# Kernel optimization log

Hardware: AMD Instinct MI355X
Metric: run time of the kernel (lower is better)

Reference implementation:

```python
import jax, jax.numpy as jnp
import numpy as np

jax.config.update("jax_enable_x64", True)  # FixedPointMul math is done in float64, as in torch

B, S, H = 8, 4096, 768


def setup_inputs():
    key = jax.random.key(0)
    k = jax.random.split(key, 6)
    s_act = jnp.array([4.0 / 127.0], dtype=jnp.float32)  # per-tensor 8-bit activation scale

    def qact(kk):  # produce int8-quantized-looking activations
        x = jax.random.normal(kk, (B, S, H), jnp.float32)
        return s_act * jnp.clip(jnp.round(x / s_act), -128, 127)

    return {
        "hidden_states": qact(k[0]),
        "hidden_states_scaling_factor": s_act,
        "input_tensor": qact(k[1]),
        "input_tensor_scaling_factor": s_act,
        "dense_weight": 0.02 * jax.random.normal(k[2], (H, H), jnp.float32),
        "dense_bias": 0.01 * jax.random.normal(k[3], (H,), jnp.float32),
        "ln_weight": 1.0 + 0.05 * jax.random.normal(k[4], (H,), jnp.float32),
        "ln_bias": 0.05 * jax.random.normal(k[5], (H,), jnp.float32),
    }


def _sym_scale(k, smin, smax):
    n = 2 ** (k - 1) - 1
    return jnp.clip(jnp.maximum(jnp.abs(smin), jnp.abs(smax)), 1e-8, None) / n


def _sym_quant(x, k, scale):
    n = 2 ** (k - 1) - 1
    return jnp.clip(jnp.round(x / scale), -n, n - 1)


def _batch_frexp(x):
    # returns (round(mantissa * 2^31), 31 - exponent) as in ibert batch_frexp
    m, e = jnp.frexp(x)
    return jnp.floor(m * (2.0 ** 31) + 0.5), 31.0 - e


def _fixedpoint_mul(x, pre_scale, bit, z_scale, identity=None, id_scale=None):
    n = 2 ** (bit - 1) - 1
    ps = jnp.reshape(pre_scale, (1, 1, -1)).astype(jnp.float64)
    z = z_scale.astype(jnp.float64)
    z_int = jnp.round(x.astype(jnp.float64) / ps)
    m, e = _batch_frexp(ps / z)
    out = jnp.round(z_int * m / (2.0 ** e))
    if identity is not None:
        isf = jnp.reshape(id_scale, (1, 1, -1)).astype(jnp.float64)
        wx = jnp.round(identity.astype(jnp.float64) / isf)
        m1, e1 = _batch_frexp(isf / z)
        out = out + jnp.round(wx * m1 / (2.0 ** e1))
    return jnp.clip(out, -n - 1, n).astype(jnp.float32)


def _quant_act(x, bit, pre_scale, identity=None, id_scale=None):
    x_act = x if identity is None else x + identity
    s = _sym_scale(bit, x_act.min(), x_act.max())  # per-tensor scale (dynamic range)
    q = _fixedpoint_mul(x, pre_scale, bit, s, identity, id_scale)
    return q * s, s


def reference(hidden_states, hidden_states_scaling_factor, input_tensor, input_tensor_scaling_factor, dense_weight, dense_bias, ln_weight, ln_bias):
    # ---- QuantLinear: per-channel int8 weights, int32 bias ----
    w_min = dense_weight.min(axis=1)
    w_max = dense_weight.max(axis=1)
    fc_scale = _sym_scale(8, w_min, w_max)                      # [H_out]
    w_int = _sym_quant(dense_weight, 8, fc_scale[:, None])      # [H_out, H_in]
    bias_scale = fc_scale * hidden_states_scaling_factor        # [H_out]
    b_int = _sym_quant(dense_bias, 32, bias_scale)
    x_int = hidden_states / hidden_states_scaling_factor
    hs = (jnp.einsum("bsh,oh->bso", x_int, w_int) + b_int) * bias_scale
    # dropout: eval mode -> identity
    # ---- QuantAct(22-bit) with quantized residual add ----
    hs, ln_in_scale = _quant_act(hs, 22, bias_scale, input_tensor, input_tensor_scaling_factor)
    # ---- IntLayerNorm (integer-only LayerNorm) ----
    x_int = hs / ln_in_scale
    mean_int = jnp.round(jnp.mean(x_int, axis=2, keepdims=True))
    y_int = x_int - mean_int
    var0 = jnp.sum(y_int ** 2, axis=2, keepdims=True)
    shift = jnp.ceil(jnp.log2(jnp.sqrt(jnp.maximum(var0, 1.0) / 2.0 ** 32)))  # set_shift (max_bit=32)
    shift = jnp.maximum(0.0, shift.max())
    y_sh = jnp.floor(y_int / 2.0 ** shift)
    var_int = jnp.sum(y_sh ** 2, axis=2, keepdims=True)
    std_int = jnp.floor(jnp.sqrt(var_int)) * 2.0 ** shift
    factor = jnp.floor(2.0 ** 31 / std_int)
    y_int = jnp.floor(y_int * factor / 2.0)
    sf = jnp.sqrt(jnp.float32(H)) / 2.0 ** 30
    bias_int = jnp.floor((ln_bias / ln_weight) / sf)
    y_int = y_int + bias_int
    sf_out = sf * ln_weight                                     # [H]
    hs = y_int * sf_out
    # ---- QuantAct(8-bit) output requantization ----
    hs, out_scale = _quant_act(hs, 8, sf_out)
    return hs, out_scale
```

## Files before the change

kernel.cpp:

```cpp
#include <hip/hip_runtime.h>

typedef int   v4i   __attribute__((ext_vector_type(4)));
typedef unsigned long u64x2 __attribute__((ext_vector_type(2)));

#define HDIM 768
#define NTOK 32768

static constexpr size_t WX_OFF   = 0;
static constexpr size_t WINT_OFF = 25165824;
static constexpr size_t RS1_OFF  = WINT_OFF + 1179648;
static constexpr size_t RS2_OFF  = RS1_OFF + 6144;
static constexpr size_t BS_OFF   = RS2_OFF + 6144;
static constexpr size_t BINT_OFF = BS_OFF + 3072;
static constexpr size_t LNBI_OFF = BINT_OFF + 3072;
static constexpr size_t SFO_OFF  = LNBI_OFF + 3072;
static constexpr size_t SC_OFF   = SFO_OFF + 3072;
static constexpr size_t RSM1_OFF = SC_OFF + 64;

__device__ __forceinline__ unsigned fenc(float f) {
    unsigned u = __float_as_uint(f);
    return (u >> 31) ? ~u : (u | 0x80000000u);
}
__device__ __forceinline__ float fdec(unsigned e) {
    unsigned u = (e >> 31) ? (e & 0x7fffffffu) : ~e;
    return __uint_as_float(u);
}

#define GLDS16(g, l) __builtin_amdgcn_global_load_lds( \
    (const __attribute__((address_space(1))) unsigned int*)(g), \
    (__attribute__((address_space(3))) unsigned int*)(l), 16, 0, 0)

__device__ __forceinline__ int swz4(int r) { return (r & 3) ^ ((r >> 2) & 3); }

__global__ __launch_bounds__(256) void k0_prep(const float* __restrict__ W,
                                               const float* __restrict__ bias,
                                               const float* __restrict__ ln_w,
                                               const float* __restrict__ ln_b,
                                               const float* __restrict__ phsf,
                                               char* __restrict__ ws) {
    int o = blockIdx.x, tid = threadIdx.x;
    __shared__ float red[256];
    __shared__ float fc_sh;
    float m = 0.f;
    for (int j = tid; j < HDIM; j += 256) m = fmaxf(m, fabsf(W[(size_t)o * HDIM + j]));
    red[tid] = m;
    __syncthreads();
    for (int s = 128; s; s >>= 1) { if (tid < s) red[tid] = fmaxf(red[tid], red[tid + s]); __syncthreads(); }
    if (tid == 0) {
        float fc = fmaxf(red[0], 1e-8f) / 127.0f;
        float hsf = *phsf;
        float bs = fc * hsf;
        fc_sh = fc;
        ((float*)(ws + BS_OFF))[o] = bs;
        ((int*)(ws + BINT_OFF))[o] = (int)rintf(bias[o] / bs);
        float sf = sqrtf(768.0f) / 1073741824.0f;
        float lw = ln_w[o], lb = ln_b[o];
        ((int*)(ws + LNBI_OFF))[o] = (int)floorf((lb / lw) / sf);
        ((float*)(ws + SFO_OFF))[o] = sf * lw;
    }
    __syncthreads();
    float fc = fc_sh;
    char* w8 = (char*)(ws + WINT_OFF);
    for (int j = tid; j < HDIM; j += 256) {
        float q = rintf(W[(size_t)o * HDIM + j] / fc);
        q = fminf(fmaxf(q, -127.f), 126.f);
        w8[(size_t)o * HDIM + j] = (char)q;
    }
    if (blockIdx.x == 0 && tid < 8) {
        unsigned* sc = (unsigned*)(ws + SC_OFF);
        unsigned v = 0u;
        if (tid == 0 || tid == 2) v = 0xFFFFFFFFu;
        sc[tid] = v;
    }
}

__global__ __launch_bounds__(256) void kp_a8(const float* __restrict__ hs,
                                             const float* __restrict__ phsf,
                                             char* __restrict__ ws) {
    int idx = blockIdx.x * 256 + threadIdx.x;
    float inv = 1.0f / *phsf;
    const float4* in4 = (const float4*)hs + (size_t)idx * 4;
    unsigned ow[4];
    #pragma unroll
    for (int j = 0; j < 4; ++j) {
        float4 v = in4[j];
        int q0 = (int)rintf(v.x * inv), q1 = (int)rintf(v.y * inv);
        int q2 = (int)rintf(v.z * inv), q3 = (int)rintf(v.w * inv);
        ow[j] = (unsigned)(q0 & 255) | ((unsigned)(q1 & 255) << 8) |
                ((unsigned)(q2 & 255) << 16) | ((unsigned)(q3 & 255) << 24);
    }
    ((uint4*)(ws + WX_OFF))[idx] = make_uint4(ow[0], ow[1], ow[2], ow[3]);
}

#define BM 128
#define BN 192
#define BK 64
#define NKT (HDIM / BK)
__global__ __launch_bounds__(256) void k1_gemm(const float* __restrict__ inp,
                                               char* __restrict__ ws,
                                               int* __restrict__ accOut) {
    __shared__ alignas(16) char As[2][BM * BK];
    __shared__ alignas(16) char Bs[2][BN * BK];
    __shared__ float rmn[4], rmx[4];
    int tid = threadIdx.x, lane = tid & 63, wave = tid >> 6;
    int wrow = lane & 15, g = lane >> 4;
    int bid = blockIdx.x;
    int xcd = bid & 7, slot = bid >> 3;
    int mtile = xcd * 32 + (slot >> 2);
    int ntile = slot & 3;
    int t0 = mtile * BM, o0 = ntile * BN;
    const char* a8 = (const char*)(ws + WX_OFF);
    const char* w8 = (const char*)(ws + WINT_OFF);

    const char* asrc[2]; const char* bsrc[3];
    int aldso[2], bldso[3];
    #pragma unroll
    for (int i = 0; i < 2; ++i) {
        int c = i * 256 + tid, r = c >> 2, s = c & 3;
        asrc[i] = a8 + (size_t)(t0 + r) * HDIM + (s ^ swz4(r)) * 16;
        aldso[i] = (i * 256 + wave * 64) * 16;
    }
    #pragma unroll
    for (int i = 0; i < 3; ++i) {
        int c = i * 256 + tid, r = c >> 2, s = c & 3;
        bsrc[i] = w8 + (size_t)(o0 + r) * HDIM + (s ^ swz4(r)) * 16;
        bldso[i] = (i * 256 + wave * 64) * 16;
    }

    int wm = wave & 1, wn = wave >> 1;
    int aofs[4], bofs[6];
    #pragma unroll
    for (int mi = 0; mi < 4; ++mi) { int r = wm * 64 + mi * 16 + wrow; aofs[mi] = r * BK + ((g ^ swz4(r)) * 16); }
    #pragma unroll
    for (int nf = 0; nf < 6; ++nf) { int r = wn * 96 + nf * 16 + wrow; bofs[nf] = r * BK + ((g ^ swz4(r)) * 16); }

    #pragma unroll
    for (int i = 0; i < 2; ++i) GLDS16(asrc[i], &As[0][aldso[i]]);
    #pragma unroll
    for (int i = 0; i < 3; ++i) GLDS16(bsrc[i], &Bs[0][bldso[i]]);
    #pragma unroll
    for (int i = 0; i < 2; ++i) GLDS16(asrc[i] + BK, &As[1][aldso[i]]);
    #pragma unroll
    for (int i = 0; i < 3; ++i) GLDS16(bsrc[i] + BK, &Bs[1][bldso[i]]);
    asm volatile("s_waitcnt vmcnt(5)" ::: "memory");
    __builtin_amdgcn_s_barrier();

    v4i acc[4][6] = {};
    for (int kt = 0; kt < NKT; ++kt) {
        int cur = kt & 1;
        u64x2 af[4], bf[6];
        #pragma unroll
        for (int mi = 0; mi < 4; ++mi) af[mi] = *(const u64x2*)&As[cur][aofs[mi]];
        #pragma unroll
        for (int nf = 0; nf < 6; ++nf) bf[nf] = *(const u64x2*)&Bs[cur][bofs[nf]];
        asm volatile("s_waitcnt lgkmcnt(0)" ::: "memory");
        __builtin_amdgcn_s_barrier();
        if (kt + 2 < NKT) {
            #pragma unroll
            for (int i = 0; i < 2; ++i) GLDS16(asrc[i] + (kt + 2) * BK, &As[cur][aldso[i]]);
            #pragma unroll
            for (int i = 0; i < 3; ++i) GLDS16(bsrc[i] + (kt + 2) * BK, &Bs[cur][bldso[i]]);
        }
        __builtin_amdgcn_s_setprio(1);
        #pragma unroll
        for (int mi = 0; mi < 4; ++mi)
            #pragma unroll
            for (int nf = 0; nf < 6; ++nf) {
                acc[mi][nf] = __builtin_amdgcn_mfma_i32_16x16x32_i8((long)af[mi][0], (long)bf[nf][0], acc[mi][nf], 0, 0, 0);
                acc[mi][nf] = __builtin_amdgcn_mfma_i32_16x16x32_i8((long)af[mi][1], (long)bf[nf][1], acc[mi][nf], 0, 0, 0);
            }
        __builtin_amdgcn_s_setprio(0);
        if (kt + 2 < NKT) {
            asm volatile("s_waitcnt vmcnt(5)" ::: "memory");
            __builtin_amdgcn_s_barrier();
        } else if (kt + 2 == NKT) {
            asm volatile("s_waitcnt vmcnt(0)" ::: "memory");
            __builtin_amdgcn_s_barrier();
        }
    }

    const float* bscale = (const float*)(ws + BS_OFF);
    const int* bint = (const int*)(ws + BINT_OFF);
    int oo[6]; float bsc[6]; int bi[6];
    #pragma unroll
    for (int nf = 0; nf < 6; ++nf) {
        oo[nf] = o0 + wn * 96 + nf * 16 + wrow;
        bsc[nf] = bscale[oo[nf]];
        bi[nf]  = bint[oo[nf]];
    }
    float lmn = 3.402823466e38f, lmx = -3.402823466e38f;
    #pragma unroll
    for (int mi = 0; mi < 4; ++mi)
        #pragma unroll
        for (int r = 0; r < 4; ++r) {
            int t = t0 + wm * 64 + mi * 16 + g * 4 + r;
            size_t rb = (size_t)t * HDIM;
            #pragma unroll
            for (int nf = 0; nf < 6; ++nf) {
                int a = acc[mi][nf][r] + bi[nf];
                size_t idx = rb + oo[nf];
                accOut[idx] = a;
                float xa = (float)a * bsc[nf] + inp[idx];
                lmn = fminf(lmn, xa);
                lmx = fmaxf(lmx, xa);
            }
        }
    #pragma unroll
    for (int off = 32; off; off >>= 1) {
        lmn = fminf(lmn, __shfl_down(lmn, off));
        lmx = fmaxf(lmx, __shfl_down(lmx, off));
    }
    if (lane == 0) { rmn[wave] = lmn; rmx[wave] = lmx; }
    __syncthreads();
    if (tid == 0) {
        float mn = fminf(fminf(rmn[0], rmn[1]), fminf(rmn[2], rmn[3]));
        float mx = fmaxf(fmaxf(rmx[0], rmx[1]), fmaxf(rmx[2], rmx[3]));
        volatile unsigned* sc = (volatile unsigned*)(ws + SC_OFF);
        unsigned emn = fenc(mn), emx = fenc(mx);
        if (emn < sc[0]) atomicMin((unsigned*)&sc[0], emn);
        if (emx > sc[1]) atomicMax((unsigned*)&sc[1], emx);
    }
}

__global__ __launch_bounds__(256) void k2_scale1(const float* __restrict__ pisf, char* __restrict__ ws) {
    __shared__ float s_sh;
    unsigned* sc = (unsigned*)(ws + SC_OFF);
    if (threadIdx.x == 0) {
        float mn = fdec(sc[0]), mx = fdec(sc[1]);
        float s = fmaxf(fmaxf(fabsf(mn), fabsf(mx)), 1e-8f) / 2097151.0f;
        ((float*)sc)[5] = s;
        s_sh = s;
        double r = (double)(*pisf) / (double)s;
        int ex; double mant = frexp(r, &ex);
        double m1 = floor(mant * 2147483648.0 + 0.5);
        ((double*)(ws + RSM1_OFF))[0] = m1 * exp2((double)(ex - 31));
    }
    __syncthreads();
    float s = s_sh;
    const float* bs = (const float*)(ws + BS_OFF);
    double* rs1 = (double*)(ws + RS1_OFF);
    for (int o = threadIdx.x; o < HDIM; o += 256) {
        double r = (double)bs[o] / (double)s;
        int ex; double mant = frexp(r, &ex);
        double m = floor(mant * 2147483648.0 + 0.5);
        rs1[o] = m * exp2((double)(ex - 31));
    }
}

__global__ __launch_bounds__(256) void k3_rows(char* __restrict__ ws, int* __restrict__ buf,
                                               const float* __restrict__ inp,
                                               const float* __restrict__ pisf) {
    int tid = threadIdx.x, lane = tid & 63, wave = tid >> 6;
    int wid = blockIdx.x * 4 + wave;
    const double* rs1 = (const double*)(ws + RS1_OFF);
    double rsm1 = *(const double*)(ws + RSM1_OFF);
    float inv_isf = 1.0f / *pisf;
    int localShift = 0;
    int4 aP[3]; float4 xP[3];
    {
        size_t b0 = (size_t)(wid * 4) * HDIM;
        #pragma unroll
        for (int c = 0; c < 3; ++c) {
            aP[c] = ((const int4*)(buf + b0))[lane + 64 * c];
            xP[c] = ((const float4*)(inp + b0))[lane + 64 * c];
        }
    }
    for (int rr = 0; rr < 4; ++rr) {
        int4 aN[3]; float4 xN[3];
        if (rr < 3) {
            size_t nb = (size_t)(wid * 4 + rr + 1) * HDIM;
            #pragma unroll
            for (int c = 0; c < 3; ++c) {
                aN[c] = ((const int4*)(buf + nb))[lane + 64 * c];
                xN[c] = ((const float4*)(inp + nb))[lane + 64 * c];
            }
        }
        size_t base = (size_t)(wid * 4 + rr) * HDIM;
        int q[12];
        int sum = 0;
        #pragma unroll
        for (int c = 0; c < 3; ++c) {
            int o0 = (lane + 64 * c) * 4;
            int av[4] = {aP[c].x, aP[c].y, aP[c].z, aP[c].w};
            float xv[4] = {xP[c].x, xP[c].y, xP[c].z, xP[c].w};
            #pragma unroll
            for (int j = 0; j < 4; ++j) {
                double q1 = rint((double)av[j] * rs1[o0 + j]);
                int wxj = (int)rintf(xv[j] * inv_isf);
                double qq = q1 + rint((double)wxj * rsm1);
                qq = fmin(fmax(qq, -2097152.0), 2097151.0);
                q[c * 4 + j] = (int)qq;
                sum += q[c * 4 + j];
            }
        }
        #pragma unroll
        for (int off = 32; off; off >>= 1) sum += __shfl_xor(sum, off);
        int mean = (int)rint((double)sum / 768.0);
        long long var0 = 0;
        #pragma unroll
        for (int k = 0; k < 12; ++k) { q[k] -= mean; var0 += (long long)q[k] * (long long)q[k]; }
        #pragma unroll
        for (int off = 32; off; off >>= 1) var0 += __shfl_xor(var0, off);
        #pragma unroll
        for (int c = 0; c < 3; ++c) {
            int4 y = {q[c * 4 + 0], q[c * 4 + 1], q[c * 4 + 2], q[c * 4 + 3]};
            ((int4*)(buf + base))[lane + 64 * c] = y;
        }
        if (lane == 0) {
            double v = (double)(var0 < 1 ? 1LL : var0);
            int sr = (int)ceil(0.5 * log2(v) - 16.0);
            localShift = max(localShift, sr);
        }
        #pragma unroll
        for (int c = 0; c < 3; ++c) { aP[c] = aN[c]; xP[c] = xN[c]; }
    }
    if (lane == 0 && localShift > 0) {
        int* sp = (int*)(ws + SC_OFF) + 4;
        if (localShift > *(volatile int*)sp) atomicMax(sp, localShift);
    }
}

__global__ __launch_bounds__(256) void k4_rows(char* __restrict__ ws, int* __restrict__ buf) {
    int tid = threadIdx.x, lane = tid & 63, wave = tid >> 6;
    int wid = blockIdx.x * 4 + wave;
    int shift = *(((const int*)(ws + SC_OFF)) + 4);
    const int* lnbi = (const int*)(ws + LNBI_OFF);
    const float* sfo = (const float*)(ws + SFO_OFF);
    float lmn = 3.402823466e38f, lmx = -3.402823466e38f;
    int4 yP[3];
    {
        size_t b0 = (size_t)(wid * 4) * HDIM;
        #pragma unroll
        for (int c = 0; c < 3; ++c) yP[c] = ((const int4*)(buf + b0))[lane + 64 * c];
    }
    for (int rr = 0; rr < 4; ++rr) {
        int4 yN[3];
        if (rr < 3) {
            size_t nb = (size_t)(wid * 4 + rr + 1) * HDIM;
            #pragma unroll
            for (int c = 0; c < 3; ++c) yN[c] = ((const int4*)(buf + nb))[lane + 64 * c];
        }
        size_t base = (size_t)(wid * 4 + rr) * HDIM;
        int yv[12];
        #pragma unroll
        for (int c = 0; c < 3; ++c) {
            yv[c * 4 + 0] = yP[c].x; yv[c * 4 + 1] = yP[c].y; yv[c * 4 + 2] = yP[c].z; yv[c * 4 + 3] = yP[c].w;
        }
        long long var = 0;
        #pragma unroll
        for (int k = 0; k < 12; ++k) { int ysh = yv[k] >> shift; var += (long long)ysh * (long long)ysh; }
        #pragma unroll
        for (int off = 32; off; off >>= 1) var += __shfl_xor(var, off);
        double std_int = floor(sqrt((double)var)) * (double)(1LL << shift);
        if (std_int < 1.0) std_int = 1.0;
        long long factor = (long long)floor(2147483648.0 / std_int);
        #pragma unroll
        for (int c = 0; c < 3; ++c) {
            int o0 = (lane + 64 * c) * 4;
            int y2[4];
            #pragma unroll
            for (int j = 0; j < 4; ++j) {
                long long t = ((long long)yv[c * 4 + j] * factor) >> 1;
                int v2 = (int)t + lnbi[o0 + j];
                y2[j] = v2;
                float h = (float)v2 * sfo[o0 + j];
                lmn = fminf(lmn, h);
                lmx = fmaxf(lmx, h);
            }
            int4 w = {y2[0], y2[1], y2[2], y2[3]};
            ((int4*)(buf + base))[lane + 64 * c] = w;
        }
        #pragma unroll
        for (int c = 0; c < 3; ++c) yP[c] = yN[c];
    }
    #pragma unroll
    for (int off = 32; off; off >>= 1) {
        lmn = fminf(lmn, __shfl_xor(lmn, off));
        lmx = fmaxf(lmx, __shfl_xor(lmx, off));
    }
    if (lane == 0) {
        volatile unsigned* sc = (volatile unsigned*)(ws + SC_OFF);
        unsigned emn = fenc(lmn), emx = fenc(lmx);
        if (emn < sc[2]) atomicMin((unsigned*)&sc[2], emn);
        if (emx > sc[3]) atomicMax((unsigned*)&sc[3], emx);
    }
}

__global__ __launch_bounds__(256) void k5_scale2(char* __restrict__ ws) {
    __shared__ float s_sh;
    unsigned* sc = (unsigned*)(ws + SC_OFF);
    if (threadIdx.x == 0) {
        float mn = fdec(sc[2]), mx = fdec(sc[3]);
        float s2 = fmaxf(fmaxf(fabsf(mn), fabsf(mx)), 1e-8f) / 127.0f;
        ((float*)sc)[6] = s2;
        s_sh = s2;
    }
    __syncthreads();
    float s2 = s_sh;
    const float* sfo = (const float*)(ws + SFO_OFF);
    double* rs2 = (double*)(ws + RS2_OFF);
    for (int o = threadIdx.x; o < HDIM; o += 256) {
        double r = (double)sfo[o] / (double)s2;
        int ex; double mant = frexp(r, &ex);
        double m = floor(mant * 2147483648.0 + 0.5);
        rs2[o] = m * exp2((double)(ex - 31));
    }
}

__global__ __launch_bounds__(256) void k6_out(char* __restrict__ ws, float* __restrict__ out) {
    int idx4 = blockIdx.x * 256 + threadIdx.x;
    int4 y = ((const int4*)out)[idx4];
    const double* rs2 = (const double*)(ws + RS2_OFF);
    float s2 = ((const float*)(ws + SC_OFF))[6];
    int base = idx4 * 4;
    int o0 = base % HDIM;
    int yv[4] = {y.x, y.y, y.z, y.w};
    float4 r;
    float* rp = &r.x;
    #pragma unroll
    for (int j = 0; j < 4; ++j) {
        double q = rint((double)yv[j] * rs2[o0 + j]);
        q = fmin(fmax(q, -128.0), 127.0);
        rp[j] = (float)q * s2;
    }
    ((float4*)out)[idx4] = r;
    if (idx4 == 0) out[(size_t)NTOK * HDIM] = s2;
}

extern "C" void kernel_launch(void* const* d_in, const int* in_sizes, int n_in,
                              void* d_out, int out_size, void* d_ws, size_t ws_size,
                              hipStream_t stream) {
    const float* hs   = (const float*)d_in[0];
    const float* phsf = (const float*)d_in[1];
    const float* inp  = (const float*)d_in[2];
    const float* pisf = (const float*)d_in[3];
    const float* W    = (const float*)d_in[4];
    const float* bias = (const float*)d_in[5];
    const float* ln_w = (const float*)d_in[6];
    const float* ln_b = (const float*)d_in[7];
    char* ws = (char*)d_ws;
    float* out = (float*)d_out;
    int* buf = (int*)d_out;

    k0_prep<<<HDIM, 256, 0, stream>>>(W, bias, ln_w, ln_b, phsf, ws);
    kp_a8<<<NTOK * HDIM / 4096, 256, 0, stream>>>(hs, phsf, ws);
    k1_gemm<<<(NTOK / BM) * (HDIM / BN), 256, 0, stream>>>(inp, ws, buf);
    k2_scale1<<<1, 256, 0, stream>>>(pisf, ws);
    k3_rows<<<NTOK / 16, 256, 0, stream>>>(ws, buf, inp, pisf);
    k4_rows<<<NTOK / 16, 256, 0, stream>>>(ws, buf);
    k5_scale2<<<1, 256, 0, stream>>>(ws);
    k6_out<<<NTOK * HDIM / 1024, 256, 0, stream>>>(ws, out);
}
```

Measured before the change: 440.1 us.

## Store per-row LN factor instead of rewriting buffer; recompute in output kernel

k4 no longer writes the normalized integer row back to the buffer. It stores one factor per row in workspace, and k6 recomputes y*factor>>1 + bias from the centered values, which removes a full-tensor write pass. k3 and k4 now handle one row per wave instead of four, with four times as many blocks. k4 also reduces min/max within the block through shared memory before issuing atomics. The trade is a little extra integer arithmetic in k6 and more blocks and atomics in k3.

```diff
diff --git a/kernel.cpp b/kernel.cpp
--- a/kernel.cpp
+++ b/kernel.cpp
@@ -8,6 +8,7 @@
 
 static constexpr size_t WX_OFF   = 0;
 static constexpr size_t WINT_OFF = 25165824;
+static constexpr size_t FACT_OFF = WINT_OFF + 589824;
 static constexpr size_t RS1_OFF  = WINT_OFF + 1179648;
 static constexpr size_t RS2_OFF  = RS1_OFF + 6144;
 static constexpr size_t BS_OFF   = RS2_OFF + 6144;
@@ -251,136 +252,107 @@
                                                const float* __restrict__ inp,
                                                const float* __restrict__ pisf) {
     int tid = threadIdx.x, lane = tid & 63, wave = tid >> 6;
-    int wid = blockIdx.x * 4 + wave;
+    int row = blockIdx.x * 4 + wave;
     const double* rs1 = (const double*)(ws + RS1_OFF);
     double rsm1 = *(const double*)(ws + RSM1_OFF);
     float inv_isf = 1.0f / *pisf;
-    int localShift = 0;
-    int4 aP[3]; float4 xP[3];
-    {
-        size_t b0 = (size_t)(wid * 4) * HDIM;
-        #pragma unroll
-        for (int c = 0; c < 3; ++c) {
-            aP[c] = ((const int4*)(buf + b0))[lane + 64 * c];
-            xP[c] = ((const float4*)(inp + b0))[lane + 64 * c];
-        }
-    }
-    for (int rr = 0; rr < 4; ++rr) {
-        int4 aN[3]; float4 xN[3];
-        if (rr < 3) {
-            size_t nb = (size_t)(wid * 4 + rr + 1) * HDIM;
-            #pragma unroll
-            for (int c = 0; c < 3; ++c) {
-                aN[c] = ((const int4*)(buf + nb))[lane + 64 * c];
-                xN[c] = ((const float4*)(inp + nb))[lane + 64 * c];
-            }
-        }
-        size_t base = (size_t)(wid * 4 + rr) * HDIM;
-        int q[12];
-        int sum = 0;
-        #pragma unroll
-        for (int c = 0; c < 3; ++c) {
-            int o0 = (lane + 64 * c) * 4;
-            int av[4] = {aP[c].x, aP[c].y, aP[c].z, aP[c].w};
-            float xv[4] = {xP[c].x, xP[c].y, xP[c].z, xP[c].w};
-            #pragma unroll
-            for (int j = 0; j < 4; ++j) {
-                double q1 = rint((double)av[j] * rs1[o0 + j]);
-                int wxj = (int)rintf(xv[j] * inv_isf);
-                double qq = q1 + rint((double)wxj * rsm1);
-                qq = fmin(fmax(qq, -2097152.0), 2097151.0);
-                q[c * 4 + j] = (int)qq;
-                sum += q[c * 4 + j];
-            }
-        }
-        #pragma unroll
-        for (int off = 32; off; off >>= 1) sum += __shfl_xor(sum, off);
-        int mean = (int)rint((double)sum / 768.0);
-        long long var0 = 0;
-        #pragma unroll
-        for (int k = 0; k < 12; ++k) { q[k] -= mean; var0 += (long long)q[k] * (long long)q[k]; }
-        #pragma unroll
-        for (int off = 32; off; off >>= 1) var0 += __shfl_xor(var0, off);
-        #pragma unroll
-        for (int c = 0; c < 3; ++c) {
-            int4 y = {q[c * 4 + 0], q[c * 4 + 1], q[c * 4 + 2], q[c * 4 + 3]};
-            ((int4*)(buf + base))[lane + 64 * c] = y;
-        }
-        if (lane == 0) {
-            double v = (double)(var0 < 1 ? 1LL : var0);
-            int sr = (int)ceil(0.5 * log2(v) - 16.0);
-            localShift = max(localShift, sr);
-        }
-        #pragma unroll
-        for (int c = 0; c < 3; ++c) { aP[c] = aN[c]; xP[c] = xN[c]; }
-    }
-    if (lane == 0 && localShift > 0) {
-        int* sp = (int*)(ws + SC_OFF) + 4;
-        if (localShift > *(volatile int*)sp) atomicMax(sp, localShift);
-    }
-}
-
-__global__ __launch_bounds__(256) void k4_rows(char* __restrict__ ws, int* __restrict__ buf) {
+    size_t base = (size_t)row * HDIM;
+    int4 a[3]; float4 x[3];
+    #pragma unroll
+    for (int c = 0; c < 3; ++c) {
+        a[c] = ((const int4*)(buf + base))[lane + 64 * c];
+        x[c] = ((const float4*)(inp + base))[lane + 64 * c];
+    }
+    int q[12];
+    int sum = 0;
+    #pragma unroll
+    for (int c = 0; c < 3; ++c) {
+        int o0 = (lane + 64 * c) * 4;
+        int av[4] = {a[c].x, a[c].y, a[c].z, a[c].w};
+        float xv[4] = {x[c].x, x[c].y, x[c].z, x[c].w};
+        #pragma unroll
+        for (int j = 0; j < 4; ++j) {
+            double q1 = rint((double)av[j] * rs1[o0 + j]);
+            int wxj = (int)rintf(xv[j] * inv_isf);
+            double qq = q1 + rint((double)wxj * rsm1);
+            qq = fmin(fmax(qq, -2097152.0), 2097151.0);
+            q[c * 4 + j] = (int)qq;
+            sum += q[c * 4 + j];
+        }
+    }
+    #pragma unroll
+    for (int off = 32; off; off >>= 1) sum += __shfl_xor(sum, off);
+    int mean = (int)rint((double)sum / 768.0);
+    long long var0 = 0;
+    #pragma unroll
+    for (int k = 0; k < 12; ++k) { q[k] -= mean; var0 += (long long)q[k] * (long long)q[k]; }
+    #pragma unroll
+    for (int off = 32; off; off >>= 1) var0 += __shfl_xor(var0, off);
+    #pragma unroll
+    for (int c = 0; c < 3; ++c) {
+        int4 y = {q[c * 4 + 0], q[c * 4 + 1], q[c * 4 + 2], q[c * 4 + 3]};
+        ((int4*)(buf + base))[lane + 64 * c] = y;
+    }
+    if (lane == 0) {
+        double v = (double)(var0 < 1 ? 1LL : var0);
+        int sr = (int)ceil(0.5 * log2(v) - 16.0);
+        if (sr > 0) {
+            int* sp = (int*)(ws + SC_OFF) + 4;
+            if (sr > *(volatile int*)sp) atomicMax(sp, sr);
+        }
+    }
+}
+
+__global__ __launch_bounds__(256) void k4_rows(char* __restrict__ ws, const int* __restrict__ buf) {
     int tid = threadIdx.x, lane = tid & 63, wave = tid >> 6;
-    int wid = blockIdx.x * 4 + wave;
+    int row = blockIdx.x * 4 + wave;
     int shift = *(((const int*)(ws + SC_OFF)) + 4);
     const int* lnbi = (const int*)(ws + LNBI_OFF);
     const float* sfo = (const float*)(ws + SFO_OFF);
+    __shared__ float rmn[4], rmx[4];
+    size_t base = (size_t)row * HDIM;
+    int4 y4[3];
+    #pragma unroll
+    for (int c = 0; c < 3; ++c) y4[c] = ((const int4*)(buf + base))[lane + 64 * c];
+    int yv[12];
+    #pragma unroll
+    for (int c = 0; c < 3; ++c) {
+        yv[c * 4 + 0] = y4[c].x; yv[c * 4 + 1] = y4[c].y; yv[c * 4 + 2] = y4[c].z; yv[c * 4 + 3] = y4[c].w;
+    }
+    long long var = 0;
+    #pragma unroll
+    for (int k = 0; k < 12; ++k) { int ysh = yv[k] >> shift; var += (long long)ysh * (long long)ysh; }
+    #pragma unroll
+    for (int off = 32; off; off >>= 1) var += __shfl_xor(var, off);
+    double std_int = floor(sqrt((double)var)) * (double)(1LL << shift);
+    if (std_int < 1.0) std_int = 1.0;
+    long long factor = (long long)floor(2147483648.0 / std_int);
+    if (lane == 0) ((unsigned*)(ws + FACT_OFF))[row] = (unsigned)factor;
     float lmn = 3.402823466e38f, lmx = -3.402823466e38f;
-    int4 yP[3];
-    {
-        size_t b0 = (size_t)(wid * 4) * HDIM;
-        #pragma unroll
-        for (int c = 0; c < 3; ++c) yP[c] = ((const int4*)(buf + b0))[lane + 64 * c];
-    }
-    for (int rr = 0; rr < 4; ++rr) {
-        int4 yN[3];
-        if (rr < 3) {
-            size_t nb = (size_t)(wid * 4 + rr + 1) * HDIM;
-            #pragma unroll
-            for (int c = 0; c < 3; ++c) yN[c] = ((const int4*)(buf + nb))[lane + 64 * c];
-        }
-        size_t base = (size_t)(wid * 4 + rr) * HDIM;
-        int yv[12];
-        #pragma unroll
-        for (int c = 0; c < 3; ++c) {
-            yv[c * 4 + 0] = yP[c].x; yv[c * 4 + 1] = yP[c].y; yv[c * 4 + 2] = yP[c].z; yv[c * 4 + 3] = yP[c].w;
-        }
-        long long var = 0;
-        #pragma unroll
-        for (int k = 0; k < 12; ++k) { int ysh = yv[k] >> shift; var += (long long)ysh * (long long)ysh; }
-        #pragma unroll
-        for (int off = 32; off; off >>= 1) var += __shfl_xor(var, off);
-        double std_int = floor(sqrt((double)var)) * (double)(1LL << shift);
-        if (std_int < 1.0) std_int = 1.0;
-        long long factor = (long long)floor(2147483648.0 / std_int);
-        #pragma unroll
-        for (int c = 0; c < 3; ++c) {
-            int o0 = (lane + 64 * c) * 4;
-            int y2[4];
-            #pragma unroll
-            for (int j = 0; j < 4; ++j) {
-                long long t = ((long long)yv[c * 4 + j] * factor) >> 1;
-                int v2 = (int)t + lnbi[o0 + j];
-                y2[j] = v2;
-                float h = (float)v2 * sfo[o0 + j];
-                lmn = fminf(lmn, h);
-                lmx = fmaxf(lmx, h);
-            }
-            int4 w = {y2[0], y2[1], y2[2], y2[3]};
-            ((int4*)(buf + base))[lane + 64 * c] = w;
-        }
-        #pragma unroll
-        for (int c = 0; c < 3; ++c) yP[c] = yN[c];
+    #pragma unroll
+    for (int c = 0; c < 3; ++c) {
+        int o0 = (lane + 64 * c) * 4;
+        #pragma unroll
+        for (int j = 0; j < 4; ++j) {
+            long long t = ((long long)yv[c * 4 + j] * factor) >> 1;
+            int v2 = (int)t + lnbi[o0 + j];
+            float h = (float)v2 * sfo[o0 + j];
+            lmn = fminf(lmn, h);
+            lmx = fmaxf(lmx, h);
+        }
     }
     #pragma unroll
     for (int off = 32; off; off >>= 1) {
         lmn = fminf(lmn, __shfl_xor(lmn, off));
         lmx = fmaxf(lmx, __shfl_xor(lmx, off));
     }
-    if (lane == 0) {
+    if (lane == 0) { rmn[wave] = lmn; rmx[wave] = lmx; }
+    __syncthreads();
+    if (tid == 0) {
+        float mn = fminf(fminf(rmn[0], rmn[1]), fminf(rmn[2], rmn[3]));
+        float mx = fmaxf(fmaxf(rmx[0], rmx[1]), fmaxf(rmx[2], rmx[3]));
         volatile unsigned* sc = (volatile unsigned*)(ws + SC_OFF);
-        unsigned emn = fenc(lmn), emx = fenc(lmx);
+        unsigned emn = fenc(mn), emx = fenc(mx);
         if (emn < sc[2]) atomicMin((unsigned*)&sc[2], emn);
         if (emx > sc[3]) atomicMax((unsigned*)&sc[3], emx);
     }
@@ -411,7 +383,9 @@
     int idx4 = blockIdx.x * 256 + threadIdx.x;
     int4 y = ((const int4*)out)[idx4];
     const double* rs2 = (const double*)(ws + RS2_OFF);
+    const int* lnbi = (const int*)(ws + LNBI_OFF);
     float s2 = ((const float*)(ws + SC_OFF))[6];
+    long long factor = (long long)((const unsigned*)(ws + FACT_OFF))[idx4 / 192];
     int base = idx4 * 4;
     int o0 = base % HDIM;
     int yv[4] = {y.x, y.y, y.z, y.w};
@@ -419,7 +393,9 @@
     float* rp = &r.x;
     #pragma unroll
     for (int j = 0; j < 4; ++j) {
-        double q = rint((double)yv[j] * rs2[o0 + j]);
+        long long t = ((long long)yv[j] * factor) >> 1;
+        int v2 = (int)t + lnbi[o0 + j];
+        double q = rint((double)v2 * rs2[o0 + j]);
         q = fmin(fmax(q, -128.0), 127.0);
         rp[j] = (float)q * s2;
     }
@@ -446,8 +422,8 @@
     kp_a8<<<NTOK * HDIM / 4096, 256, 0, stream>>>(hs, phsf, ws);
     k1_gemm<<<(NTOK / BM) * (HDIM / BN), 256, 0, stream>>>(inp, ws, buf);
     k2_scale1<<<1, 256, 0, stream>>>(pisf, ws);
-    k3_rows<<<NTOK / 16, 256, 0, stream>>>(ws, buf, inp, pisf);
-    k4_rows<<<NTOK / 16, 256, 0, stream>>>(ws, buf);
+    k3_rows<<<NTOK / 4, 256, 0, stream>>>(ws, buf, inp, pisf);
+    k4_rows<<<NTOK / 4, 256, 0, stream>>>(ws, buf);
     k5_scale2<<<1, 256, 0, stream>>>(ws);
     k6_out<<<NTOK * HDIM / 1024, 256, 0, stream>>>(ws, out);
 }
```

After: 469.2 us. +6.6%, slower.

## Drop k4 row writeback by storing per-row factor and recomputing in output kernel

Applied to the files above, without the earlier changes.

k4 no longer writes the normalized int rows back to the buffer. It only stores the per-row LayerNorm factor in the workspace and computes min/max. k6 is restructured to process whole rows per wave, recomputing y*factor+bias before requantizing, which removes one full-tensor write. Per-lane parameter tables are hoisted into registers in k3, k4 and k6, and k4's min/max atomics are reduced per block through shared memory. The trade is extra integer arithmetic in k6 and more register pressure.

```diff
diff --git a/kernel.cpp b/kernel.cpp
--- a/kernel.cpp
+++ b/kernel.cpp
@@ -8,6 +8,7 @@
 
 static constexpr size_t WX_OFF   = 0;
 static constexpr size_t WINT_OFF = 25165824;
+static constexpr size_t FACT_OFF = WINT_OFF + 589824;
 static constexpr size_t RS1_OFF  = WINT_OFF + 1179648;
 static constexpr size_t RS2_OFF  = RS1_OFF + 6144;
 static constexpr size_t BS_OFF   = RS2_OFF + 6144;
@@ -255,6 +256,13 @@
     const double* rs1 = (const double*)(ws + RS1_OFF);
     double rsm1 = *(const double*)(ws + RSM1_OFF);
     float inv_isf = 1.0f / *pisf;
+    double t_rs1[12];
+    #pragma unroll
+    for (int c = 0; c < 3; ++c) {
+        int o0 = (lane + 64 * c) * 4;
+        #pragma unroll
+        for (int j = 0; j < 4; ++j) t_rs1[c * 4 + j] = rs1[o0 + j];
+    }
     int localShift = 0;
     int4 aP[3]; float4 xP[3];
     {
@@ -280,12 +288,11 @@
         int sum = 0;
         #pragma unroll
         for (int c = 0; c < 3; ++c) {
-            int o0 = (lane + 64 * c) * 4;
             int av[4] = {aP[c].x, aP[c].y, aP[c].z, aP[c].w};
             float xv[4] = {xP[c].x, xP[c].y, xP[c].z, xP[c].w};
             #pragma unroll
             for (int j = 0; j < 4; ++j) {
-                double q1 = rint((double)av[j] * rs1[o0 + j]);
+                double q1 = rint((double)av[j] * t_rs1[c * 4 + j]);
                 int wxj = (int)rintf(xv[j] * inv_isf);
                 double qq = q1 + rint((double)wxj * rsm1);
                 qq = fmin(fmax(qq, -2097152.0), 2097151.0);
@@ -320,12 +327,21 @@
     }
 }
 
-__global__ __launch_bounds__(256) void k4_rows(char* __restrict__ ws, int* __restrict__ buf) {
+__global__ __launch_bounds__(256) void k4_rows(char* __restrict__ ws, const int* __restrict__ buf) {
     int tid = threadIdx.x, lane = tid & 63, wave = tid >> 6;
     int wid = blockIdx.x * 4 + wave;
     int shift = *(((const int*)(ws + SC_OFF)) + 4);
     const int* lnbi = (const int*)(ws + LNBI_OFF);
     const float* sfo = (const float*)(ws + SFO_OFF);
+    __shared__ float rmn[4], rmx[4];
+    int t_lnbi[12]; float t_sfo[12];
+    #pragma unroll
+    for (int c = 0; c < 3; ++c) {
+        int o0 = (lane + 64 * c) * 4;
+        #pragma unroll
+        for (int j = 0; j < 4; ++j) { t_lnbi[c * 4 + j] = lnbi[o0 + j]; t_sfo[c * 4 + j] = sfo[o0 + j]; }
+    }
+    unsigned* fact = (unsigned*)(ws + FACT_OFF);
     float lmn = 3.402823466e38f, lmx = -3.402823466e38f;
     int4 yP[3];
     {
@@ -340,7 +356,6 @@
             #pragma unroll
             for (int c = 0; c < 3; ++c) yN[c] = ((const int4*)(buf + nb))[lane + 64 * c];
         }
-        size_t base = (size_t)(wid * 4 + rr) * HDIM;
         int yv[12];
         #pragma unroll
         for (int c = 0; c < 3; ++c) {
@@ -354,21 +369,14 @@
         double std_int = floor(sqrt((double)var)) * (double)(1LL << shift);
         if (std_int < 1.0) std_int = 1.0;
         long long factor = (long long)floor(2147483648.0 / std_int);
-        #pragma unroll
-        for (int c = 0; c < 3; ++c) {
-            int o0 = (lane + 64 * c) * 4;
-            int y2[4];
-            #pragma unroll
-            for (int j = 0; j < 4; ++j) {
-                long long t = ((long long)yv[c * 4 + j] * factor) >> 1;
-                int v2 = (int)t + lnbi[o0 + j];
-                y2[j] = v2;
-                float h = (float)v2 * sfo[o0 + j];
-                lmn = fminf(lmn, h);
-                lmx = fmaxf(lmx, h);
-            }
-            int4 w = {y2[0], y2[1], y2[2], y2[3]};
-            ((int4*)(buf + base))[lane + 64 * c] = w;
+        if (lane == 0) fact[wid * 4 + rr] = (unsigned)factor;
+        #pragma unroll
+        for (int k = 0; k < 12; ++k) {
+            long long t = ((long long)yv[k] * factor) >> 1;
+            int v2 = (int)t + t_lnbi[k];
+            float h = (float)v2 * t_sfo[k];
+            lmn = fminf(lmn, h);
+            lmx = fmaxf(lmx, h);
         }
         #pragma unroll
         for (int c = 0; c < 3; ++c) yP[c] = yN[c];
@@ -378,9 +386,13 @@
         lmn = fminf(lmn, __shfl_xor(lmn, off));
         lmx = fmaxf(lmx, __shfl_xor(lmx, off));
     }
-    if (lane == 0) {
+    if (lane == 0) { rmn[wave] = lmn; rmx[wave] = lmx; }
+    __syncthreads();
+    if (tid == 0) {
+        float mn = fminf(fminf(rmn[0], rmn[1]), fminf(rmn[2], rmn[3]));
+        float mx = fmaxf(fmaxf(rmx[0], rmx[1]), fmaxf(rmx[2], rmx[3]));
         volatile unsigned* sc = (volatile unsigned*)(ws + SC_OFF);
-        unsigned emn = fenc(lmn), emx = fenc(lmx);
+        unsigned emn = fenc(mn), emx = fenc(mx);
         if (emn < sc[2]) atomicMin((unsigned*)&sc[2], emn);
         if (emx > sc[3]) atomicMax((unsigned*)&sc[3], emx);
     }
@@ -408,23 +420,59 @@
 }
 
 __global__ __launch_bounds__(256) void k6_out(char* __restrict__ ws, float* __restrict__ out) {
-    int idx4 = blockIdx.x * 256 + threadIdx.x;
-    int4 y = ((const int4*)out)[idx4];
+    int tid = threadIdx.x, lane = tid & 63, wave = tid >> 6;
+    int wid = blockIdx.x * 4 + wave;
     const double* rs2 = (const double*)(ws + RS2_OFF);
+    const int* lnbi = (const int*)(ws + LNBI_OFF);
+    const unsigned* fact = (const unsigned*)(ws + FACT_OFF);
     float s2 = ((const float*)(ws + SC_OFF))[6];
-    int base = idx4 * 4;
-    int o0 = base % HDIM;
-    int yv[4] = {y.x, y.y, y.z, y.w};
-    float4 r;
-    float* rp = &r.x;
-    #pragma unroll
-    for (int j = 0; j < 4; ++j) {
-        double q = rint((double)yv[j] * rs2[o0 + j]);
-        q = fmin(fmax(q, -128.0), 127.0);
-        rp[j] = (float)q * s2;
-    }
-    ((float4*)out)[idx4] = r;
-    if (idx4 == 0) out[(size_t)NTOK * HDIM] = s2;
+    double t_rs2[12]; int t_lnbi[12];
+    #pragma unroll
+    for (int c = 0; c < 3; ++c) {
+        int o0 = (lane + 64 * c) * 4;
+        #pragma unroll
+        for (int j = 0; j < 4; ++j) { t_rs2[c * 4 + j] = rs2[o0 + j]; t_lnbi[c * 4 + j] = lnbi[o0 + j]; }
+    }
+    int* buf = (int*)out;
+    int4 yP[3];
+    {
+        size_t b0 = (size_t)(wid * 4) * HDIM;
+        #pragma unroll
+        for (int c = 0; c < 3; ++c) yP[c] = ((const int4*)(buf + b0))[lane + 64 * c];
+    }
+    for (int rr = 0; rr < 4; ++rr) {
+        int4 yN[3];
+        if (rr < 3) {
+            size_t nb = (size_t)(wid * 4 + rr + 1) * HDIM;
+            #pragma unroll
+            for (int c = 0; c < 3; ++c) yN[c] = ((const int4*)(buf + nb))[lane + 64 * c];
+        }
+        size_t base = (size_t)(wid * 4 + rr) * HDIM;
+        long long factor = (long long)fact[wid * 4 + rr];
+        int yv[12];
+        #pragma unroll
+        for (int c = 0; c < 3; ++c) {
+            yv[c * 4 + 0] = yP[c].x; yv[c * 4 + 1] = yP[c].y; yv[c * 4 + 2] = yP[c].z; yv[c * 4 + 3] = yP[c].w;
+        }
+        #pragma unroll
+        for (int c = 0; c < 3; ++c) {
+            float4 r;
+            float* rp = &r.x;
+            #pragma unroll
+            for (int j = 0; j < 4; ++j) {
+                int k = c * 4 + j;
+                long long t = ((long long)yv[k] * factor) >> 1;
+                int v2 = (int)t + t_lnbi[k];
+                double q = rint((double)v2 * t_rs2[k]);
+                q = fmin(fmax(q, -128.0), 127.0);
+                rp[j] = (float)q * s2;
+            }
+            ((float4*)(out + base))[lane + 64 * c] = r;
+        }
+        #pragma unroll
+        for (int c = 0; c < 3; ++c) yP[c] = yN[c];
+    }
+    if (wid == 0 && tid == 0) out[(size_t)NTOK * HDIM] = s2;
 }
 
 extern "C" void kernel_launch(void* const* d_in, const int* in_sizes, int n_in,
@@ -449,5 +497,5 @@
     k3_rows<<<NTOK / 16, 256, 0, stream>>>(ws, buf, inp, pisf);
     k4_rows<<<NTOK / 16, 256, 0, stream>>>(ws, buf);
     k5_scale2<<<1, 256, 0, stream>>>(ws);
-    k6_out<<<NTOK * HDIM / 1024, 256, 0, stream>>>(ws, out);
-}
+    k6_out<<<NTOK / 16, 256, 0, stream>>>(ws, out);
+}
```

Result: faster. 412.7 us (-6.2%).
